# Performance work log

Hardware: AMD Instinct MI355X
Metric: run time of the kernel (lower is better)

The kernel has to match this reference:

```python
import jax, jax.numpy as jnp
import numpy as np

N_EMBD = 1024

def setup_inputs() -> dict:
    key = jax.random.key(0)
    ks = jax.random.split(key, 7)
    x = jax.random.normal(ks[0], (4, 2048, N_EMBD), dtype=jnp.float32)
    s = 1.0 / np.sqrt(N_EMBD)
    Wk = jax.random.normal(ks[1], (N_EMBD, N_EMBD), dtype=jnp.float32) * s
    bk = jnp.zeros((N_EMBD,), dtype=jnp.float32)
    Wq = jax.random.normal(ks[2], (N_EMBD, N_EMBD), dtype=jnp.float32) * s
    bq = jnp.zeros((N_EMBD,), dtype=jnp.float32)
    Wv = jax.random.normal(ks[3], (N_EMBD, N_EMBD), dtype=jnp.float32) * s
    bv = jnp.zeros((N_EMBD,), dtype=jnp.float32)
    return {"x": x, "Wk": Wk, "bk": bk, "Wq": Wq, "bq": bq, "Wv": Wv, "bv": bv}

def reference(x, Wk, bk, Wq, bq, Wv, bv):
    B, T, C = x.shape
    k = x @ Wk.T + bk  # [B,T,C]
    q = x @ Wq.T + bq
    v = x @ Wv.T + bv
    # scaled scores with causal mask (note: original scales by C**-0.5)
    scores = jnp.einsum('btc,bsc->bts', q, k) * (C ** -0.5)  # [B,T,T]
    causal = jnp.tril(jnp.ones((T, T), dtype=bool))
    scores = jnp.where(causal, scores, -jnp.inf)
    weights = jax.nn.softmax(scores, axis=-1)
    # dropout disabled (inference mode)
    y = jnp.einsum('bts,bsc->btc', weights, v)
    return y
```

## Files before the change

kernel.cpp:

```cpp
#include <hip/hip_runtime.h>
#include <hip/hip_bf16.h>

typedef __attribute__((ext_vector_type(8))) short short8;
typedef __attribute__((ext_vector_type(4))) float f32x4;

__device__ __forceinline__ ushort f2b(float f) {
    __hip_bfloat16 h = __float2bfloat16(f);
    return *reinterpret_cast<ushort*>(&h);
}
__device__ __forceinline__ float b2f(ushort u) {
    return __uint_as_float(((unsigned)u) << 16);
}
__device__ __forceinline__ void gload16(const ushort* g, ushort* l) {
    __builtin_amdgcn_global_load_lds(
        (const __attribute__((address_space(1))) void*)g,
        (__attribute__((address_space(3))) void*)l, 16, 0, 0);
}

__global__ __launch_bounds__(512, 1) void qkv_gemm256(
    const ushort* __restrict__ xb, const ushort* __restrict__ Wcat,
    const float* __restrict__ bk, const float* __restrict__ bq, const float* __restrict__ bv,
    ushort* __restrict__ Kb, ushort* __restrict__ Qb, ushort* __restrict__ Vt) {
    constexpr int T = 2048, C = 1024, K = 1024, NT = 16;
    __shared__ ushort smem[49152];

    const int tid = threadIdx.x;
    const int l = tid & 63, w = tid >> 6;
    const int wm = (w >> 1) * 64, wn = (w & 1) * 64;
    const int lr = l & 15, lk = l >> 4;

    const int b = blockIdx.x;
    const int wg = (b & 7) * 96 + (b >> 3);
    const int m0 = (wg / 24) * 256, n0 = (wg % 24) * 128;

    const int srow = w * 16 + (l >> 2);
    const int scb = ((l & 3) << 4) ^ ((l & 32) ? 32 : 0);
    const ushort* gA = xb + (size_t)(m0 + srow) * K + (scb >> 1);
    const ushort* gB = Wcat + (size_t)(n0 + srow) * K + (scb >> 1);

    const int LB = lr * 32 + ((lk << 3) ^ ((lr >= 8) ? 16 : 0));

    f32x4 acc[4][4] = {};

#define STAGEQ(u1, ks)                                                    \
    {                                                                     \
        ushort* _base = smem + ((u1) & 1) * 24576 + (ks) * 12288;         \
        const int _ko = (u1) * 64 + (ks) * 32;                            \
        ushort* _da = _base + w * 512;                                    \
        gload16(gA + _ko, _da);                                           \
        gload16(gA + (size_t)128 * K + _ko, _da + 4096);                  \
        gload16(gB + _ko, _base + 8192 + w * 512);                        \
    }

    STAGEQ(0, 0);
    STAGEQ(0, 1);

    for (int u = 0; u < NT; ++u) {
        const ushort* buf = smem + (u & 1) * 24576;
        asm volatile("s_waitcnt vmcnt(3)" ::: "memory");
        __builtin_amdgcn_s_barrier();
        asm volatile("" ::: "memory");
        {
            const ushort* Ab = buf + (wm >> 4) * 512 + LB;
            const ushort* Bb = buf + 8192 + (wn >> 4) * 512 + LB;
            short8 af[4], bf4[4];
#pragma unroll
            for (int f = 0; f < 4; ++f) af[f] = *reinterpret_cast<const short8*>(Ab + f * 512);
#pragma unroll
            for (int g = 0; g < 4; ++g) bf4[g] = *reinterpret_cast<const short8*>(Bb + g * 512);
            if (u + 1 < NT) STAGEQ(u + 1, 0);
            __builtin_amdgcn_s_setprio(1);
#pragma unroll
            for (int f = 0; f < 4; ++f)
#pragma unroll
                for (int g = 0; g < 4; ++g)
                    acc[f][g] = __builtin_amdgcn_mfma_f32_16x16x32_bf16(af[f], bf4[g], acc[f][g], 0, 0, 0);
            __builtin_amdgcn_s_setprio(0);
        }
        if (u + 1 < NT) asm volatile("s_waitcnt vmcnt(3)" ::: "memory");
        else            asm volatile("s_waitcnt vmcnt(0)" ::: "memory");
        __builtin_amdgcn_s_barrier();
        asm volatile("" ::: "memory");
        {
            const ushort* Ab = buf + 12288 + (wm >> 4) * 512 + LB;
            const ushort* Bb = buf + 12288 + 8192 + (wn >> 4) * 512 + LB;
            short8 af[4], bf4[4];
#pragma unroll
            for (int f = 0; f < 4; ++f) af[f] = *reinterpret_cast<const short8*>(Ab + f * 512);
#pragma unroll
            for (int g = 0; g < 4; ++g) bf4[g] = *reinterpret_cast<const short8*>(Bb + g * 512);
            if (u + 1 < NT) STAGEQ(u + 1, 1);
            __builtin_amdgcn_s_setprio(1);
#pragma unroll
            for (int f = 0; f < 4; ++f)
#pragma unroll
                for (int g = 0; g < 4; ++g)
                    acc[f][g] = __builtin_amdgcn_mfma_f32_16x16x32_bf16(af[f], bf4[g], acc[f][g], 0, 0, 0);
            __builtin_amdgcn_s_setprio(0);
        }
    }
#undef STAGEQ

    const int zsel = n0 >> 10;
    const int c0 = (n0 & 1023) + wn;
    if (zsel < 2) {
        ushort* O = (zsel == 0) ? Kb : Qb;
        const float* bias = (zsel == 0) ? bk : bq;
#pragma unroll
        for (int f = 0; f < 4; ++f)
#pragma unroll
            for (int g = 0; g < 4; ++g) {
                const int gc = c0 + g * 16 + lr;
                const float badd = bias[gc];
#pragma unroll
                for (int rr = 0; rr < 4; ++rr) {
                    const int gr = m0 + wm + f * 16 + lk * 4 + rr;
                    O[(size_t)gr * C + gc] = f2b(acc[f][g][rr] + badd);
                }
            }
    } else {
        const int zb = (m0 + wm) >> 11;
        const int s0 = (m0 + wm) & 2047;
        ushort* Vz = Vt + (size_t)zb * C * T;
#pragma unroll
        for (int f = 0; f < 4; ++f)
#pragma unroll
            for (int g = 0; g < 4; ++g) {
                const int gc = c0 + g * 16 + lr;
                const float badd = bv[gc];
                const int s = s0 + f * 16 + lk * 4;
                ushort tmp[4];
#pragma unroll
                for (int rr = 0; rr < 4; ++rr) tmp[rr] = f2b(acc[f][g][rr] + badd);
                *reinterpret_cast<uint2*>(Vz + (size_t)gc * T + s) =
                    *reinterpret_cast<uint2*>(tmp);
            }
    }
}

template <int MODE>
__global__ __launch_bounds__(256, 3) void gemm_ring(
    const ushort* __restrict__ Kb, const ushort* __restrict__ Qb,
    const ushort* __restrict__ Vt, ushort* __restrict__ Sb, float* __restrict__ out) {
    constexpr int T = 2048, C = 1024;
    __shared__ ushort smem[24576];

    const int tid = threadIdx.x;
    const int l = tid & 63, w = tid >> 6;
    const int wm = (w >> 1) * 64, wn = (w & 1) * 64;
    const int lr = l & 15, lk = l >> 4;

    int m0, n0, nt, iblk = 0, jblk = 0, z = 0;
    const ushort *Au, *Bu;
    int ldA, ldB;
    if constexpr (MODE == 1) {
        const int wg0 = blockIdx.x;
        const int wg = (wg0 & 7) * 68 + (wg0 >> 3);
        z = wg / 136; const int t136 = wg % 136;
        int i = (int)((sqrtf(8.f * t136 + 1.f) - 1.f) * 0.5f);
        while ((i + 1) * (i + 2) / 2 <= t136) ++i;
        while (i * (i + 1) / 2 > t136) --i;
        const int j = t136 - i * (i + 1) / 2;
        iblk = i; jblk = j;
        m0 = i * 128; n0 = j * 128;
        Au = Qb + (size_t)z * T * C + (size_t)m0 * C; ldA = C;
        Bu = Kb + (size_t)z * T * C + (size_t)n0 * C; ldB = C;
        nt = 32;
    } else {
        const int wg0 = blockIdx.x;
        const int wg = (wg0 & 7) * 64 + (wg0 >> 3);
        const int half = wg >> 8, s2 = wg & 255;
        z = s2 >> 6; const int r6 = s2 & 63;
        const int nb = r6 & 7, ii = r6 >> 3;
        const int i = half ? (15 - ii) : ii;
        iblk = i;
        m0 = i * 128; n0 = nb * 128;
        Au = Sb + (size_t)z * T * T + (size_t)m0 * T; ldA = T;
        Bu = Vt + (size_t)z * C * T + (size_t)n0 * T; ldB = T;
        nt = 4 * (i + 1);
    }

    const int srow = w * 16 + (l >> 2);
    const int scb = ((l & 3) << 4) ^ ((l >= 32) ? 32 : 0);
    const ushort* gA = Au + (size_t)srow * ldA + (scb >> 1);
    const ushort* gB = Bu + (size_t)srow * ldB + (scb >> 1);
    const size_t a64 = (size_t)64 * ldA, b64 = (size_t)64 * ldB;
    const int LBu = lr * 32 + ((lk << 3) ^ ((lr >= 8) ? 16 : 0));

    f32x4 acc[4][4] = {};
    f32x4 acc1[4] = {};
    short8 ones;
#pragma unroll
    for (int q = 0; q < 8; ++q) ones[q] = (short)0x3F80;

#define STAGE(tt, sl)                                                    \
    {                                                                    \
        const int _ko = (tt) * 32;                                       \
        ushort* _d = smem + (sl) * 8192 + w * 512;                       \
        gload16(gA + _ko,        _d);                                    \
        gload16(gA + a64 + _ko,  _d + 2048);                             \
        gload16(gB + _ko,        _d + 4096);                             \
        gload16(gB + b64 + _ko,  _d + 6144);                             \
    }

    STAGE(0, 0);
    STAGE(1, 1);
    asm volatile("s_waitcnt vmcnt(4)" ::: "memory");
    __builtin_amdgcn_s_barrier();
    asm volatile("" ::: "memory");

    int sc = 0, ss = 2;
    for (int t = 0; t < nt; ++t) {
        const ushort* As = smem + sc * 8192 + (wm >> 4) * 512 + LBu;
        const ushort* Bs = smem + sc * 8192 + 4096 + (wn >> 4) * 512 + LBu;
        short8 af[4], bf[4];
#pragma unroll
        for (int q = 0; q < 4; ++q) {
            af[q] = *reinterpret_cast<const short8*>(As + q * 512);
            bf[q] = *reinterpret_cast<const short8*>(Bs + q * 512);
        }
        if (t + 2 < nt) STAGE(t + 2, ss);
        __builtin_amdgcn_s_setprio(1);
#pragma unroll
        for (int mf = 0; mf < 4; ++mf)
#pragma unroll
            for (int nf = 0; nf < 4; ++nf)
                acc[mf][nf] = __builtin_amdgcn_mfma_f32_16x16x32_bf16(af[mf], bf[nf], acc[mf][nf], 0, 0, 0);
        if constexpr (MODE == 2) {
#pragma unroll
            for (int mf = 0; mf < 4; ++mf)
                acc1[mf] = __builtin_amdgcn_mfma_f32_16x16x32_bf16(af[mf], ones, acc1[mf], 0, 0, 0);
        }
        __builtin_amdgcn_s_setprio(0);
        if (t + 1 < nt) {
            if (t + 2 < nt) asm volatile("s_waitcnt vmcnt(4)" ::: "memory");
            else            asm volatile("s_waitcnt vmcnt(0)" ::: "memory");
            __builtin_amdgcn_s_barrier();
            asm volatile("" ::: "memory");
        }
        sc = (sc == 2) ? 0 : sc + 1;
        ss = (ss == 2) ? 0 : ss + 1;
    }
#undef STAGE

    if constexpr (MODE == 1) {
        ushort* Sp = Sb + (size_t)z * T * T;
        const bool diag = (iblk == jblk);
#pragma unroll
        for (int mf = 0; mf < 4; ++mf)
#pragma unroll
            for (int nf = 0; nf < 4; ++nf) {
                const int gc = n0 + wn + nf * 16 + lr;
#pragma unroll
                for (int rr = 0; rr < 4; ++rr) {
                    const int gr = m0 + wm + mf * 16 + lk * 4 + rr;
                    float p = __expf(acc[mf][nf][rr] * 0.03125f);
                    if (diag && gc > gr) p = 0.f;
                    Sp[(size_t)gr * T + gc] = f2b(p);
                }
            }
    } else {
        float* Op = out + (size_t)z * T * C;
#pragma unroll
        for (int mf = 0; mf < 4; ++mf)
#pragma unroll
            for (int rr = 0; rr < 4; ++rr) {
                const int gr = m0 + wm + mf * 16 + lk * 4 + rr;
                const float inv = 1.0f / acc1[mf][rr];
#pragma unroll
                for (int nf = 0; nf < 4; ++nf) {
                    const int gc = n0 + wn + nf * 16 + lr;
                    Op[(size_t)gr * C + gc] = acc[mf][nf][rr] * inv;
                }
            }
    }
}

__global__ __launch_bounds__(256) void cvt_all(
    const float* __restrict__ x, const float* __restrict__ Wk,
    const float* __restrict__ Wq, const float* __restrict__ Wv,
    ushort* __restrict__ xb, ushort* __restrict__ Wcat) {
    constexpr int C = 1024;
    constexpr int NX = 8388608 / 8, NW = C * C / 8;
    int i = blockIdx.x * 256 + threadIdx.x;
    const float* src; ushort* dst;
    if (i < NX)               { src = x;  dst = xb; }
    else if (i < NX + NW)     { src = Wk; dst = Wcat;                 i -= NX; }
    else if (i < NX + 2 * NW) { src = Wq; dst = Wcat + (size_t)C * C; i -= NX + NW; }
    else                      { src = Wv; dst = Wcat + 2 * (size_t)C * C; i -= NX + 2 * NW; }
    const float4* p = reinterpret_cast<const float4*>(src) + (size_t)i * 2;
    float4 a = p[0], b = p[1];
    ushort o[8] = {f2b(a.x), f2b(a.y), f2b(a.z), f2b(a.w),
                   f2b(b.x), f2b(b.y), f2b(b.z), f2b(b.w)};
    reinterpret_cast<uint4*>(dst)[i] = *reinterpret_cast<uint4*>(o);
}

extern "C" void kernel_launch(void* const* d_in, const int* in_sizes, int n_in,
                              void* d_out, int out_size, void* d_ws, size_t ws_size,
                              hipStream_t stream) {
    const float* x  = (const float*)d_in[0];
    const float* Wk = (const float*)d_in[1];
    const float* bk = (const float*)d_in[2];
    const float* Wq = (const float*)d_in[3];
    const float* bq = (const float*)d_in[4];
    const float* Wv = (const float*)d_in[5];
    const float* bv = (const float*)d_in[6];
    float* out = (float*)d_out;

    constexpr int B = 4, T = 2048, C = 1024;
    constexpr size_t BTC = (size_t)B * T * C;

    ushort* Kb = (ushort*)d_ws;
    ushort* Qb = Kb + BTC;
    ushort* Vt = Qb + BTC;
    ushort* Sb = Vt + BTC;
    ushort* xb   = Sb;
    ushort* Wcat = Sb + BTC;

    dim3 blk(256);

    cvt_all<<<dim3(5632), blk, 0, stream>>>(x, Wk, Wq, Wv, xb, Wcat);

    qkv_gemm256<<<dim3(768), dim3(512), 0, stream>>>(xb, Wcat, bk, bq, bv, Kb, Qb, Vt);

    gemm_ring<1><<<dim3(544), blk, 0, stream>>>(Kb, Qb, Vt, Sb, out);

    gemm_ring<2><<<dim3(512), blk, 0, stream>>>(Kb, Qb, Vt, Sb, out);
}
```

Measured before the change: 137.0 us.

## Switch QKV GEMM to three-slot ring buffer with one barrier per k-step

Replaces the two-buffer, two-half-step pipeline in the QKV projection GEMM with a three-slot ring of 32-wide k-slices. Each iteration prefetches two slices ahead and needs only one barrier. This cuts LDS use from 96KB to 72KB and raises the launch-bounds occupancy hint to 4, aiming for more resident blocks and fewer synchronisation points. The hint could force register limits that conflict with the 64-float accumulator per thread.

```diff
diff --git a/kernel.cpp b/kernel.cpp
--- a/kernel.cpp
+++ b/kernel.cpp
@@ -17,12 +17,12 @@
         (__attribute__((address_space(3))) void*)l, 16, 0, 0);
 }
 
-__global__ __launch_bounds__(512, 1) void qkv_gemm256(
+__global__ __launch_bounds__(512, 4) void qkv_gemm256(
     const ushort* __restrict__ xb, const ushort* __restrict__ Wcat,
     const float* __restrict__ bk, const float* __restrict__ bq, const float* __restrict__ bv,
     ushort* __restrict__ Kb, ushort* __restrict__ Qb, ushort* __restrict__ Vt) {
-    constexpr int T = 2048, C = 1024, K = 1024, NT = 16;
-    __shared__ ushort smem[49152];
+    constexpr int T = 2048, C = 1024, K = 1024, NT = 32;
+    __shared__ ushort smem[36864];
 
     const int tid = threadIdx.x;
     const int l = tid & 63, w = tid >> 6;
@@ -42,62 +42,47 @@
 
     f32x4 acc[4][4] = {};
 
-#define STAGEQ(u1, ks)                                                    \
+#define STAGEQ(tt, sl)                                                    \
     {                                                                     \
-        ushort* _base = smem + ((u1) & 1) * 24576 + (ks) * 12288;         \
-        const int _ko = (u1) * 64 + (ks) * 32;                            \
-        ushort* _da = _base + w * 512;                                    \
-        gload16(gA + _ko, _da);                                           \
-        gload16(gA + (size_t)128 * K + _ko, _da + 4096);                  \
-        gload16(gB + _ko, _base + 8192 + w * 512);                        \
+        const int _ko = (tt) * 32;                                        \
+        ushort* _s = smem + (sl) * 12288 + w * 512;                       \
+        gload16(gA + _ko,                   _s);                          \
+        gload16(gA + (size_t)128 * K + _ko, _s + 4096);                   \
+        gload16(gB + _ko,                   _s + 8192);                   \
     }
 
     STAGEQ(0, 0);
-    STAGEQ(0, 1);
-
-    for (int u = 0; u < NT; ++u) {
-        const ushort* buf = smem + (u & 1) * 24576;
-        asm volatile("s_waitcnt vmcnt(3)" ::: "memory");
-        __builtin_amdgcn_s_barrier();
-        asm volatile("" ::: "memory");
-        {
-            const ushort* Ab = buf + (wm >> 4) * 512 + LB;
-            const ushort* Bb = buf + 8192 + (wn >> 4) * 512 + LB;
-            short8 af[4], bf4[4];
-#pragma unroll
-            for (int f = 0; f < 4; ++f) af[f] = *reinterpret_cast<const short8*>(Ab + f * 512);
-#pragma unroll
-            for (int g = 0; g < 4; ++g) bf4[g] = *reinterpret_cast<const short8*>(Bb + g * 512);
-            if (u + 1 < NT) STAGEQ(u + 1, 0);
-            __builtin_amdgcn_s_setprio(1);
-#pragma unroll
-            for (int f = 0; f < 4; ++f)
-#pragma unroll
-                for (int g = 0; g < 4; ++g)
-                    acc[f][g] = __builtin_amdgcn_mfma_f32_16x16x32_bf16(af[f], bf4[g], acc[f][g], 0, 0, 0);
-            __builtin_amdgcn_s_setprio(0);
+    STAGEQ(1, 1);
+    asm volatile("s_waitcnt vmcnt(3)" ::: "memory");
+    __builtin_amdgcn_s_barrier();
+    asm volatile("" ::: "memory");
+
+    int sc = 0, ss = 2;
+    for (int t = 0; t < NT; ++t) {
+        const ushort* slot = smem + sc * 12288;
+        const ushort* Ab = slot + (wm >> 4) * 512 + LB;
+        const ushort* Bb = slot + 8192 + (wn >> 4) * 512 + LB;
+        short8 af[4], bf4[4];
+#pragma unroll
+        for (int f = 0; f < 4; ++f) af[f] = *reinterpret_cast<const short8*>(Ab + f * 512);
+#pragma unroll
+        for (int g = 0; g < 4; ++g) bf4[g] = *reinterpret_cast<const short8*>(Bb + g * 512);
+        if (t + 2 < NT) STAGEQ(t + 2, ss);
+        __builtin_amdgcn_s_setprio(1);
+#pragma unroll
+        for (int f = 0; f < 4; ++f)
+#pragma unroll
+            for (int g = 0; g < 4; ++g)
+                acc[f][g] = __builtin_amdgcn_mfma_f32_16x16x32_bf16(af[f], bf4[g], acc[f][g], 0, 0, 0);
+        __builtin_amdgcn_s_setprio(0);
+        if (t + 1 < NT) {
+            if (t + 2 < NT) asm volatile("s_waitcnt vmcnt(3)" ::: "memory");
+            else            asm volatile("s_waitcnt vmcnt(0)" ::: "memory");
+            __builtin_amdgcn_s_barrier();
+            asm volatile("" ::: "memory");
         }
-        if (u + 1 < NT) asm volatile("s_waitcnt vmcnt(3)" ::: "memory");
-        else            asm volatile("s_waitcnt vmcnt(0)" ::: "memory");
-        __builtin_amdgcn_s_barrier();
-        asm volatile("" ::: "memory");
-        {
-            const ushort* Ab = buf + 12288 + (wm >> 4) * 512 + LB;
-            const ushort* Bb = buf + 12288 + 8192 + (wn >> 4) * 512 + LB;
-            short8 af[4], bf4[4];
-#pragma unroll
-            for (int f = 0; f < 4; ++f) af[f] = *reinterpret_cast<const short8*>(Ab + f * 512);
-#pragma unroll
-            for (int g = 0; g < 4; ++g) bf4[g] = *reinterpret_cast<const short8*>(Bb + g * 512);
-            if (u + 1 < NT) STAGEQ(u + 1, 1);
-            __builtin_amdgcn_s_setprio(1);
-#pragma unroll
-            for (int f = 0; f < 4; ++f)
-#pragma unroll
-                for (int g = 0; g < 4; ++g)
-                    acc[f][g] = __builtin_amdgcn_mfma_f32_16x16x32_bf16(af[f], bf4[g], acc[f][g], 0, 0, 0);
-            __builtin_amdgcn_s_setprio(0);
-        }
+        sc = (sc == 2) ? 0 : sc + 1;
+        ss = (ss == 2) ? 0 : ss + 1;
     }
 #undef STAGEQ
 
```

Measured after the change: 136.8 us (median of 2 runs). Within noise of the previous version (-0.1%).
